# Optimization experiments

Measured on AMD Instinct MI355X. Metric: run time of the kernel, lower is better.

Reference implementation:

```python
import jax, jax.numpy as jnp
import numpy as np

# Static config (matches init_kwargs / docstring example)
SHAPES = ((100, 100), (50, 50), (25, 25), (13, 13))  # (H, W) per level
L, P, NH, HD, E, F = 4, 4, 8, 32, 256, 1024
NUM_LAYERS = 6
EPS = 1e-5
NUM_KEYS = sum(h * w for h, w in SHAPES)  # 13294


def _ln(x, g, b):
    m = jnp.mean(x, -1, keepdims=True)
    v = jnp.var(x, -1, keepdims=True)
    return (x - m) * jax.lax.rsqrt(v + EPS) * g + b


def _ms_deform_attn(value, loc, aw):
    # value: (B,N,NH,HD)  loc: (B,N,NH,L,P,2) normalized  aw: (B,N,NH,L,P)
    B, N = value.shape[:2]
    out = jnp.zeros((B, NH, N, HD), value.dtype)
    start = 0
    for lvl, (h, w) in enumerate(SHAPES):
        v = value[:, start:start + h * w].transpose(0, 2, 1, 3)  # (B,NH,hw,HD)
        start += h * w
        # grid_sample align_corners=False pixel coords
        x = loc[:, :, :, lvl, :, 0] * w - 0.5  # (B,N,NH,P)
        y = loc[:, :, :, lvl, :, 1] * h - 0.5
        x0 = jnp.floor(x); y0 = jnp.floor(y)
        lx = x - x0; ly = y - y0
        x0 = x0.astype(jnp.int32); y0 = y0.astype(jnp.int32)

        def gather(yi, xi):
            valid = ((xi >= 0) & (xi < w) & (yi >= 0) & (yi < h)).astype(value.dtype)
            idx = jnp.clip(yi, 0, h - 1) * w + jnp.clip(xi, 0, w - 1)  # (B,N,NH,P)
            idx = idx.transpose(0, 2, 1, 3).reshape(B, NH, N * P, 1)
            got = jnp.take_along_axis(v, idx, axis=2).reshape(B, NH, N, P, HD)
            return got * valid.transpose(0, 2, 1, 3)[..., None]

        def wgt(a):  # (B,N,NH,P) -> (B,NH,N,P,1)
            return a.transpose(0, 2, 1, 3)[..., None]

        samp = (gather(y0, x0) * wgt((1 - lx) * (1 - ly))
                + gather(y0, x0 + 1) * wgt(lx * (1 - ly))
                + gather(y0 + 1, x0) * wgt((1 - lx) * ly)
                + gather(y0 + 1, x0 + 1) * wgt(lx * ly))  # (B,NH,N,P,HD)
        out = out + jnp.sum(samp * wgt(aw[:, :, :, lvl]), axis=3)
    return out.transpose(0, 2, 1, 3).reshape(B, N, NH * HD)


def _layer(x, ref, Woff, boff, Waw, baw, Wv, bv, Wo, bo, ln1_g, ln1_b, Wf1, bf1, Wf2, bf2, ln2_g, ln2_b):
    B, N, _ = x.shape
    v = (x @ Wv + bv).reshape(B, N, NH, HD)
    off = (x @ Woff + boff).reshape(B, N, NH, L, P, 2)
    aw = jax.nn.softmax((x @ Waw + baw).reshape(B, N, NH, L * P), -1).reshape(B, N, NH, L, P)
    normalizer = jnp.asarray([[w, h] for (h, w) in SHAPES], x.dtype)  # (L,2) in (x,y)=(W,H)
    loc = ref[:, :, None, :, None, :] + off / normalizer[None, None, None, :, None, :]
    attn = _ms_deform_attn(v, loc, aw) @ Wo + bo
    x = _ln(x + attn, ln1_g, ln1_b)
    f = jax.nn.relu(x @ Wf1 + bf1) @ Wf2 + bf2
    return _ln(x + f, ln2_g, ln2_b)


def setup_inputs() -> dict:
    key = jax.random.key(0)
    ks = jax.random.split(key, 10)
    s = 0.02
    return {
        "src": jax.random.normal(ks[0], (2, NUM_KEYS, E), jnp.float32),
        "reference_points": jax.random.uniform(ks[1], (2, NUM_KEYS, L, 2), jnp.float32),
        "spatial_shapes": jnp.asarray(SHAPES, jnp.int32),
        "level_start_index": jnp.asarray([0, 10000, 12500, 13125], jnp.int32),
        "Woff": jax.random.normal(ks[2], (E, NH * L * P * 2), jnp.float32) * s,
        "boff": jnp.zeros((NH * L * P * 2,), jnp.float32),
        "Waw": jax.random.normal(ks[3], (E, NH * L * P), jnp.float32) * s,
        "baw": jnp.zeros((NH * L * P,), jnp.float32),
        "Wv": jax.random.normal(ks[4], (E, E), jnp.float32) * s,
        "bv": jnp.zeros((E,), jnp.float32),
        "Wo": jax.random.normal(ks[5], (E, E), jnp.float32) * s,
        "bo": jnp.zeros((E,), jnp.float32),
        "ln1_g": jnp.ones((E,), jnp.float32),
        "ln1_b": jnp.zeros((E,), jnp.float32),
        "Wf1": jax.random.normal(ks[6], (E, F), jnp.float32) * s,
        "bf1": jnp.zeros((F,), jnp.float32),
        "Wf2": jax.random.normal(ks[7], (F, E), jnp.float32) * s,
        "bf2": jnp.zeros((E,), jnp.float32),
        "ln2_g": jnp.ones((E,), jnp.float32),
        "ln2_b": jnp.zeros((E,), jnp.float32),
    }


def reference(src, reference_points, spatial_shapes, level_start_index, Woff, boff, Waw, baw, Wv, bv, Wo, bo, ln1_g, ln1_b, Wf1, bf1, Wf2, bf2, ln2_g, ln2_b):
    # NOTE: the torch encoder reuses the SAME layer object num_layers times,
    # so parameters are shared across all 6 layers.
    x = src
    for _ in range(NUM_LAYERS):
        x = _layer(x, reference_points, Woff, boff, Waw, baw, Wv, bv, Wo, bo,
                   ln1_g, ln1_b, Wf1, bf1, Wf2, bf2, ln2_g, ln2_b)
    return x
```

## Files before the change

kernel.cpp:

```cpp
#include <hip/hip_runtime.h>
#include <hip/hip_bf16.h>
#include <math.h>

#define NKEYS 13294
#define BATCH 2
#define MROWS (BATCH * NKEYS)
#define EDIM  256
#define FDIM  1024
#define EPSV  1e-5f

typedef __bf16 bf16x8 __attribute__((ext_vector_type(8)));
typedef float  f32x4  __attribute__((ext_vector_type(4)));
typedef float  f32x2  __attribute__((ext_vector_type(2)));

__device__ __forceinline__ void async16(const void* g, void* l) {
    __builtin_amdgcn_global_load_lds(
        (const __attribute__((address_space(1))) void*)g,
        (__attribute__((address_space(3))) void*)l, 16, 0, 0);
}

template<int MODE>
__global__ __launch_bounds__(256, 4) void gemm_mfma_k(
    const __hip_bfloat16* __restrict__ A, const __hip_bfloat16* __restrict__ WT,
    const float* __restrict__ bias, __hip_bfloat16* __restrict__ Cout,
    int M, int N, int K,
    __hip_bfloat16* __restrict__ o_vb, __hip_bfloat16* __restrict__ o_off,
    __hip_bfloat16* __restrict__ o_aw)
{
    constexpr int BM = 128, BN = 128, BKc = 32;
    constexpr int SMX = (BM + BN) * BKc;
    __shared__ __hip_bfloat16 smem[2 * SMX];

    const int gx = gridDim.x, nb = gx * gridDim.y;
    int bxi = blockIdx.x, byi = blockIdx.y;
    if ((nb & 7) == 0) {
        const int id   = byi * gx + bxi;
        const int tile = (id & 7) * (nb >> 3) + (id >> 3);
        bxi = tile % gx; byi = tile / gx;
    }
    const int bm = byi * BM;
    const int bn = bxi * BN;

    const int tid  = threadIdx.x;
    const int lane = tid & 63;
    const int w    = tid >> 6;
    const int wr   = w >> 1, wc = w & 1;
    const int l15  = lane & 15, quad = lane >> 4;

    const int gRow = tid >> 2;
    const int kc8  = (tid & 3) * 8;
    const __hip_bfloat16* gsrc[4];
    int ldsoff[4];
    #pragma unroll
    for (int rr = 0; rr < 4; ++rr) {
        const int gr = gRow + 64 * rr;
        if (gr < BM) {
            int ar = bm + gr; if (ar >= M) ar = M - 1;
            gsrc[rr] = A + (size_t)ar * K + kc8;
        } else {
            gsrc[rr] = WT + (size_t)(bn + gr - BM) * K + kc8;
        }
        ldsoff[rr] = gr * BKc + kc8;
    }

    f32x4 acc[4][4];
    #pragma unroll
    for (int i = 0; i < 4; ++i)
        #pragma unroll
        for (int j = 0; j < 4; ++j) acc[i][j] = (f32x4)0.f;

    const int T = K / BKc;
    #pragma unroll
    for (int rr = 0; rr < 4; ++rr) async16(gsrc[rr], smem + ldsoff[rr]);

    for (int it = 0; it < T; ++it) {
        __syncthreads();
        if (it + 1 < T) {
            const int nxt = ((it + 1) & 1) * SMX;
            const int ko  = (it + 1) * BKc;
            #pragma unroll
            for (int rr = 0; rr < 4; ++rr) async16(gsrc[rr] + ko, smem + nxt + ldsoff[rr]);
        }
        const __hip_bfloat16* sA = smem + (it & 1) * SMX;
        const __hip_bfloat16* sB = sA + BM * BKc;

        bf16x8 a[4], b[4];
        #pragma unroll
        for (int mt = 0; mt < 4; ++mt)
            a[mt] = *(const bf16x8*)&sA[(wr * 64 + mt * 16 + l15) * BKc + quad * 8];
        #pragma unroll
        for (int nt = 0; nt < 4; ++nt)
            b[nt] = *(const bf16x8*)&sB[(wc * 64 + nt * 16 + l15) * BKc + quad * 8];
        #pragma unroll
        for (int mt = 0; mt < 4; ++mt)
            #pragma unroll
            for (int nt = 0; nt < 4; ++nt)
                acc[mt][nt] = __builtin_amdgcn_mfma_f32_16x16x32_bf16(
                    b[nt], a[mt], acc[mt][nt], 0, 0, 0);
    }

    #pragma unroll
    for (int nt = 0; nt < 4; ++nt) {
        const int col = bn + wc * 64 + nt * 16 + quad * 4;
        const float4 bz = *(const float4*)&bias[col];
        #pragma unroll
        for (int mt = 0; mt < 4; ++mt) {
            const int row = bm + wr * 64 + mt * 16 + l15;
            if (row >= M) continue;
            float v0 = acc[mt][nt][0] + bz.x;
            float v1 = acc[mt][nt][1] + bz.y;
            float v2 = acc[mt][nt][2] + bz.z;
            float v3 = acc[mt][nt][3] + bz.w;
            if (MODE == 3) {
                v0 = fmaxf(v0, 0.f); v1 = fmaxf(v1, 0.f);
                v2 = fmaxf(v2, 0.f); v3 = fmaxf(v3, 0.f);
            }
            union { uint2 u; __hip_bfloat16 h[4]; } p;
            p.h[0] = __float2bfloat16(v0); p.h[1] = __float2bfloat16(v1);
            p.h[2] = __float2bfloat16(v2); p.h[3] = __float2bfloat16(v3);
            if (MODE == 1) {
                if (col < 256) {
                    const int bb = (row >= NKEYS) ? 1 : 0;
                    const int hh = col >> 5, d = col & 31;
                    *(uint2*)&o_vb[((size_t)(bb * 7 + hh) * NKEYS + row) * 32 + d] = p.u;
                } else if (col < 512) {
                    *(uint2*)&o_off[(size_t)row * 256 + (col - 256)] = p.u;
                } else {
                    *(uint2*)&o_aw[(size_t)row * 128 + (col - 512)] = p.u;
                }
            } else {
                *(uint2*)&Cout[(size_t)row * N + col] = p.u;
            }
        }
    }
}

template<int FINAL>
__global__ __launch_bounds__(256, 2) void gemm_ln_k(
    const __hip_bfloat16* __restrict__ A, const __hip_bfloat16* __restrict__ WT,
    const float* __restrict__ bias, const __hip_bfloat16* __restrict__ xres,
    const float* __restrict__ g, const float* __restrict__ bta,
    float* __restrict__ xfout, __hip_bfloat16* __restrict__ xbout,
    int M, int K)
{
    constexpr int BM = 64, BN = 256, BKc = 32;
    constexpr int ROWS = BM + BN;
    constexpr int SMX = ROWS * BKc;
    __shared__ __hip_bfloat16 smem[2 * SMX];

    const int tid  = threadIdx.x;
    const int bm   = blockIdx.x * BM;
    const int lane = tid & 63;
    const int w    = tid >> 6;
    const int l15  = lane & 15, quad = lane >> 4;

    const int gRow = tid >> 2;
    const int kc8  = (tid & 3) * 8;
    const __hip_bfloat16* gsrc[5];
    int ldsoff[5];
    #pragma unroll
    for (int rr = 0; rr < 5; ++rr) {
        const int gr = gRow + 64 * rr;
        if (gr < BM) {
            int ar = bm + gr; if (ar >= M) ar = M - 1;
            gsrc[rr] = A + (size_t)ar * K + kc8;
        } else {
            gsrc[rr] = WT + (size_t)(gr - BM) * K + kc8;
        }
        ldsoff[rr] = gr * BKc + kc8;
    }

    f32x4 acc[4][4];
    #pragma unroll
    for (int i = 0; i < 4; ++i)
        #pragma unroll
        for (int j = 0; j < 4; ++j) acc[i][j] = (f32x4)0.f;

    const int T = K / BKc;
    #pragma unroll
    for (int rr = 0; rr < 5; ++rr) async16(gsrc[rr], smem + ldsoff[rr]);

    for (int it = 0; it < T; ++it) {
        __syncthreads();
        if (it + 1 < T) {
            const int nxt = ((it + 1) & 1) * SMX;
            const int ko  = (it + 1) * BKc;
            #pragma unroll
            for (int rr = 0; rr < 5; ++rr) async16(gsrc[rr] + ko, smem + nxt + ldsoff[rr]);
        }
        const __hip_bfloat16* sA = smem + (it & 1) * SMX;
        const __hip_bfloat16* sB = sA + BM * BKc;

        bf16x8 a[4], b[4];
        #pragma unroll
        for (int mt = 0; mt < 4; ++mt)
            a[mt] = *(const bf16x8*)&sA[(mt * 16 + l15) * BKc + quad * 8];
        #pragma unroll
        for (int nt = 0; nt < 4; ++nt)
            b[nt] = *(const bf16x8*)&sB[(w * 64 + nt * 16 + l15) * BKc + quad * 8];
        #pragma unroll
        for (int mt = 0; mt < 4; ++mt)
            #pragma unroll
            for (int nt = 0; nt < 4; ++nt)
                acc[mt][nt] = __builtin_amdgcn_mfma_f32_16x16x32_bf16(
                    b[nt], a[mt], acc[mt][nt], 0, 0, 0);
    }

    const int colq = w * 64 + quad * 4;

    #pragma unroll
    for (int nt = 0; nt < 4; ++nt) {
        const int col = colq + nt * 16;
        const float4 bz = *(const float4*)&bias[col];
        #pragma unroll
        for (int mt = 0; mt < 4; ++mt) {
            int row = bm + mt * 16 + l15;
            if (row >= M) row = M - 1;
            const ushort4 xr = *(const ushort4*)&xres[(size_t)row * 256 + col];
            acc[mt][nt][0] += bz.x + __uint_as_float((unsigned)xr.x << 16);
            acc[mt][nt][1] += bz.y + __uint_as_float((unsigned)xr.y << 16);
            acc[mt][nt][2] += bz.z + __uint_as_float((unsigned)xr.z << 16);
            acc[mt][nt][3] += bz.w + __uint_as_float((unsigned)xr.w << 16);
        }
    }

    __syncthreads();
    float* stats = (float*)smem;
    #pragma unroll
    for (int mt = 0; mt < 4; ++mt) {
        float s = 0.f, sq = 0.f;
        #pragma unroll
        for (int nt = 0; nt < 4; ++nt)
            #pragma unroll
            for (int r = 0; r < 4; ++r) {
                const float v = acc[mt][nt][r];
                s += v; sq += v * v;
            }
        s  += __shfl_xor(s,  16, 64);  s  += __shfl_xor(s,  32, 64);
        sq += __shfl_xor(sq, 16, 64);  sq += __shfl_xor(sq, 32, 64);
        if (quad == 0) {
            const int rl = mt * 16 + l15;
            stats[(w * 64 + rl) * 2 + 0] = s;
            stats[(w * 64 + rl) * 2 + 1] = sq;
        }
    }
    __syncthreads();

    #pragma unroll
    for (int mt = 0; mt < 4; ++mt) {
        const int rl  = mt * 16 + l15;
        const int row = bm + rl;
        float s  = stats[rl * 2]          + stats[(64 + rl) * 2]
                 + stats[(128 + rl) * 2]  + stats[(192 + rl) * 2];
        float sq = stats[rl * 2 + 1]      + stats[(64 + rl) * 2 + 1]
                 + stats[(128 + rl) * 2 + 1] + stats[(192 + rl) * 2 + 1];
        const float mean = s * (1.f / 256.f);
        const float var  = sq * (1.f / 256.f) - mean * mean;
        const float rstd = rsqrtf(var + EPSV);
        if (row < M) {
            #pragma unroll
            for (int nt = 0; nt < 4; ++nt) {
                const int col = colq + nt * 16;
                const float4 gz  = *(const float4*)&g[col];
                const float4 bb4 = *(const float4*)&bta[col];
                const float v0 = (acc[mt][nt][0] - mean) * rstd * gz.x + bb4.x;
                const float v1 = (acc[mt][nt][1] - mean) * rstd * gz.y + bb4.y;
                const float v2 = (acc[mt][nt][2] - mean) * rstd * gz.z + bb4.z;
                const float v3 = (acc[mt][nt][3] - mean) * rstd * gz.w + bb4.w;
                union { uint2 u; __hip_bfloat16 h[4]; } p;
                p.h[0] = __float2bfloat16(v0); p.h[1] = __float2bfloat16(v1);
                p.h[2] = __float2bfloat16(v2); p.h[3] = __float2bfloat16(v3);
                *(uint2*)&xbout[(size_t)row * 256 + col] = p.u;
                if (FINAL) {
                    float4 f; f.x = v0; f.y = v1; f.z = v2; f.w = v3;
                    *(float4*)&xfout[(size_t)row * 256 + col] = f;
                }
            }
        }
    }
}

__global__ void convert_wt_k(const float* __restrict__ W, __hip_bfloat16* __restrict__ WT,
                             int K, int N, int rowOff)
{
    const int idx = blockIdx.x * 256 + threadIdx.x;
    if (idx >= K * N) return;
    const int k = idx / N, n = idx % N;
    WT[(size_t)(rowOff + n) * K + k] = __float2bfloat16(W[idx]);
}

__global__ void pack_bias_k(const float* __restrict__ bv, const float* __restrict__ boff,
                            const float* __restrict__ baw, float* __restrict__ dst)
{
    const int i = blockIdx.x * 256 + threadIdx.x;
    if (i < 256) dst[i] = bv[i];
    else if (i < 512) dst[i] = boff[i - 256];
    else if (i < 640) dst[i] = baw[i - 512];
}

__global__ void convert_src_k(const float* __restrict__ src, __hip_bfloat16* __restrict__ xb)
{
    const int i = blockIdx.x * 256 + threadIdx.x;
    const float4 v = ((const float4*)src)[i];
    xb[i * 4 + 0] = __float2bfloat16(v.x);
    xb[i * 4 + 1] = __float2bfloat16(v.y);
    xb[i * 4 + 2] = __float2bfloat16(v.z);
    xb[i * 4 + 3] = __float2bfloat16(v.w);
}

__global__ __launch_bounds__(256) void sample_k(
    const __hip_bfloat16* __restrict__ v_bf,
    const __hip_bfloat16* __restrict__ offb,
    const __hip_bfloat16* __restrict__ awb,
    const float* __restrict__ ref,
    __hip_bfloat16* __restrict__ out)
{
    __shared__ alignas(16) float sw[272][4];
    __shared__ alignas(16) int   sa[272][4];
    const int t  = threadIdx.x;
    const int q0 = blockIdx.x * 2;
    const int qi = t >> 7, h = (t >> 4) & 7;

    {
        const int i = t & 15;
        const int q = q0 + qi;
        const int l = i >> 2;
        const float logit = __bfloat162float(awb[(size_t)q * 128 + h * 16 + i]);
        float mx = logit;
        #pragma unroll
        for (int m = 1; m < 16; m <<= 1) mx = fmaxf(mx, __shfl_xor(mx, m, 64));
        const float e = __expf(logit - mx);
        float s = e;
        #pragma unroll
        for (int m = 1; m < 16; m <<= 1) s += __shfl_xor(s, m, 64);
        const float aw = e / s;

        const int ww = (l == 0) ? 100 : (l == 1) ? 50 : (l == 2) ? 25 : 13;
        const int ls = (l == 0) ? 0 : (l == 1) ? 10000 : (l == 2) ? 12500 : 13125;
        const int b  = (q >= NKEYS) ? 1 : 0;
        const int slab = (b * 8 + h) * NKEYS + ls;

        const __hip_bfloat162 ofp = *(const __hip_bfloat162*)&offb[(size_t)q * 256 + h * 32 + i * 2];
        const float2 rf = *(const float2*)&ref[(size_t)q * 8 + l * 2];
        const float x = rf.x * (float)ww + __bfloat162float(ofp.x) - 0.5f;
        const float y = rf.y * (float)ww + __bfloat162float(ofp.y) - 0.5f;
        const float x0f = floorf(x), y0f = floorf(y);
        const float lx = x - x0f, ly = y - y0f;
        const int x0 = (int)x0f, y0 = (int)y0f;
        const bool x0ok = (x0 >= 0) & (x0 < ww);
        const bool x1ok = (x0 + 1 >= 0) & (x0 + 1 < ww);
        const bool y0ok = (y0 >= 0) & (y0 < ww);
        const bool y1ok = (y0 + 1 >= 0) & (y0 + 1 < ww);

        float w00 = (1.f - lx) * (1.f - ly) * aw;
        float w01 = lx * (1.f - ly) * aw;
        float w10 = (1.f - lx) * ly * aw;
        float w11 = lx * ly * aw;
        int a00 = slab + y0 * ww + x0;
        int a01 = a00 + 1;
        int a10 = a00 + ww;
        int a11 = a10 + 1;
        if (!(y0ok & x0ok)) { w00 = 0.f; a00 = 0; }
        if (!(y0ok & x1ok)) { w01 = 0.f; a01 = 0; }
        if (!(y1ok & x0ok)) { w10 = 0.f; a10 = 0; }
        if (!(y1ok & x1ok)) { w11 = 0.f; a11 = 0; }

        const int idx = (qi * 8 + h) * 17 + i;
        sw[idx][0] = w00; sw[idx][1] = w01; sw[idx][2] = w10; sw[idx][3] = w11;
        sa[idx][0] = a00 * 64; sa[idx][1] = a01 * 64;
        sa[idx][2] = a10 * 64; sa[idx][3] = a11 * 64;
    }
    __syncthreads();

    const int d2 = t & 15;
    const unsigned d4 = d2 * 4;
    const char* vb = (const char*)v_bf;
    const int ebase = (qi * 8 + h) * 17;
    f32x2 acc = (f32x2)0.f;
    #pragma unroll
    for (int i = 0; i < 16; ++i) {
        const f32x4 wv = *(const f32x4*)sw[ebase + i];
        const int4  av = *(const int4*)sa[ebase + i];
        const unsigned p0 = *(const unsigned*)(vb + ((unsigned)av.x + d4));
        const unsigned p1 = *(const unsigned*)(vb + ((unsigned)av.y + d4));
        const unsigned p2 = *(const unsigned*)(vb + ((unsigned)av.z + d4));
        const unsigned p3 = *(const unsigned*)(vb + ((unsigned)av.w + d4));
        f32x2 v;
        v[0] = __uint_as_float(p0 << 16); v[1] = __uint_as_float(p0 & 0xffff0000u);
        acc += (f32x2)(wv[0]) * v;
        v[0] = __uint_as_float(p1 << 16); v[1] = __uint_as_float(p1 & 0xffff0000u);
        acc += (f32x2)(wv[1]) * v;
        v[0] = __uint_as_float(p2 << 16); v[1] = __uint_as_float(p2 & 0xffff0000u);
        acc += (f32x2)(wv[2]) * v;
        v[0] = __uint_as_float(p3 << 16); v[1] = __uint_as_float(p3 & 0xffff0000u);
        acc += (f32x2)(wv[3]) * v;
    }
    __hip_bfloat162 ov;
    ov.x = __float2bfloat16(acc[0]);
    ov.y = __float2bfloat16(acc[1]);
    *(__hip_bfloat162*)&out[(size_t)(q0 + qi) * 256 + h * 32 + d2 * 2] = ov;
}

extern "C" void kernel_launch(void* const* d_in, const int* in_sizes, int n_in,
                              void* d_out, int out_size, void* d_ws, size_t ws_size,
                              hipStream_t stream)
{
    const float* src  = (const float*)d_in[0];
    const float* ref  = (const float*)d_in[1];
    const float* Woff = (const float*)d_in[4];
    const float* boff = (const float*)d_in[5];
    const float* Waw  = (const float*)d_in[6];
    const float* baw  = (const float*)d_in[7];
    const float* Wv   = (const float*)d_in[8];
    const float* bv   = (const float*)d_in[9];
    const float* Wo   = (const float*)d_in[10];
    const float* bo   = (const float*)d_in[11];
    const float* ln1g = (const float*)d_in[12];
    const float* ln1b = (const float*)d_in[13];
    const float* Wf1  = (const float*)d_in[14];
    const float* bf1  = (const float*)d_in[15];
    const float* Wf2  = (const float*)d_in[16];
    const float* bf2  = (const float*)d_in[17];
    const float* ln2g = (const float*)d_in[18];
    const float* ln2b = (const float*)d_in[19];

    float* x = (float*)d_out;

    float* ws = (float*)d_ws;
    float* bias1 = ws;
    __hip_bfloat16* v_bf  = (__hip_bfloat16*)(bias1 + 640);
    __hip_bfloat16* offb  = v_bf  + (size_t)MROWS * 256;
    __hip_bfloat16* awb   = offb  + (size_t)MROWS * 256;
    __hip_bfloat16* xb    = awb   + (size_t)MROWS * 128;
    __hip_bfloat16* attnb = xb    + (size_t)MROWS * 256;
    __hip_bfloat16* hb    = attnb + (size_t)MROWS * 256;
    __hip_bfloat16* WT1   = hb    + (size_t)MROWS * 1024;
    __hip_bfloat16* WTo   = WT1   + 640 * 256;
    __hip_bfloat16* WTf1  = WTo   + 256 * 256;
    __hip_bfloat16* WTf2  = WTf1  + 1024 * 256;

    convert_wt_k<<<(256 * 256 + 255) / 256, 256, 0, stream>>>(Wv,   WT1,  256, 256,   0);
    convert_wt_k<<<(256 * 256 + 255) / 256, 256, 0, stream>>>(Woff, WT1,  256, 256, 256);
    convert_wt_k<<<(256 * 128 + 255) / 256, 256, 0, stream>>>(Waw,  WT1,  256, 128, 512);
    convert_wt_k<<<(256 * 256 + 255) / 256, 256, 0, stream>>>(Wo,   WTo,  256, 256,   0);
    convert_wt_k<<<(256 * 1024 + 255) / 256, 256, 0, stream>>>(Wf1, WTf1, 256, 1024,  0);
    convert_wt_k<<<(1024 * 256 + 255) / 256, 256, 0, stream>>>(Wf2, WTf2, 1024, 256,  0);
    pack_bias_k<<<3, 256, 0, stream>>>(bv, boff, baw, bias1);
    convert_src_k<<<(MROWS * 64 + 255) / 256, 256, 0, stream>>>(src, xb);

    const int gy  = (MROWS + 127) / 128;
    const int gln = (MROWS + 63) / 64;
    for (int layer = 0; layer < 6; ++layer) {
        gemm_mfma_k<1><<<dim3(640 / 128, gy), 256, 0, stream>>>(
            xb, WT1, bias1, nullptr, MROWS, 640, 256, v_bf, offb, awb);
        sample_k<<<MROWS / 2, 256, 0, stream>>>(v_bf, offb, awb, ref, attnb);
        gemm_ln_k<0><<<gln, 256, 0, stream>>>(
            attnb, WTo, bo, xb, ln1g, ln1b, nullptr, xb, MROWS, 256);
        gemm_mfma_k<3><<<dim3(1024 / 128, gy), 256, 0, stream>>>(
            xb, WTf1, bf1, hb, MROWS, 1024, 256, nullptr, nullptr, nullptr);
        if (layer < 5)
            gemm_ln_k<0><<<gln, 256, 0, stream>>>(
                hb, WTf2, bf2, xb, ln2g, ln2b, nullptr, xb, MROWS, 1024);
        else
            gemm_ln_k<1><<<gln, 256, 0, stream>>>(
                hb, WTf2, bf2, xb, ln2g, ln2b, x, xb, MROWS, 1024);
    }
}
```

Measured before the change: 1.049 ms.

## Fuse FFN up-projection, ReLU, down-projection and LayerNorm into one kernel

Replaces the separate FFN1 GEMM (which wrote a 1024-wide hidden buffer) and the FFN2 GEMM+LN kernel with one kernel per 64-row tile. It computes 64-column chunks of the hidden activation into double-buffered LDS and immediately accumulates them into the 256-wide output, then applies the residual and LayerNorm. This removes the large hidden tensor's global write and read. In exchange, each block streams both weight matrices directly from global memory without LDS staging, and it runs with lower occupancy (launch bounds 2) and a sync per chunk.

```diff
diff --git a/kernel.cpp b/kernel.cpp
--- a/kernel.cpp
+++ b/kernel.cpp
@@ -226,6 +226,173 @@
 
     __syncthreads();
     float* stats = (float*)smem;
+    #pragma unroll
+    for (int mt = 0; mt < 4; ++mt) {
+        float s = 0.f, sq = 0.f;
+        #pragma unroll
+        for (int nt = 0; nt < 4; ++nt)
+            #pragma unroll
+            for (int r = 0; r < 4; ++r) {
+                const float v = acc[mt][nt][r];
+                s += v; sq += v * v;
+            }
+        s  += __shfl_xor(s,  16, 64);  s  += __shfl_xor(s,  32, 64);
+        sq += __shfl_xor(sq, 16, 64);  sq += __shfl_xor(sq, 32, 64);
+        if (quad == 0) {
+            const int rl = mt * 16 + l15;
+            stats[(w * 64 + rl) * 2 + 0] = s;
+            stats[(w * 64 + rl) * 2 + 1] = sq;
+        }
+    }
+    __syncthreads();
+
+    #pragma unroll
+    for (int mt = 0; mt < 4; ++mt) {
+        const int rl  = mt * 16 + l15;
+        const int row = bm + rl;
+        float s  = stats[rl * 2]          + stats[(64 + rl) * 2]
+                 + stats[(128 + rl) * 2]  + stats[(192 + rl) * 2];
+        float sq = stats[rl * 2 + 1]      + stats[(64 + rl) * 2 + 1]
+                 + stats[(128 + rl) * 2 + 1] + stats[(192 + rl) * 2 + 1];
+        const float mean = s * (1.f / 256.f);
+        const float var  = sq * (1.f / 256.f) - mean * mean;
+        const float rstd = rsqrtf(var + EPSV);
+        if (row < M) {
+            #pragma unroll
+            for (int nt = 0; nt < 4; ++nt) {
+                const int col = colq + nt * 16;
+                const float4 gz  = *(const float4*)&g[col];
+                const float4 bb4 = *(const float4*)&bta[col];
+                const float v0 = (acc[mt][nt][0] - mean) * rstd * gz.x + bb4.x;
+                const float v1 = (acc[mt][nt][1] - mean) * rstd * gz.y + bb4.y;
+                const float v2 = (acc[mt][nt][2] - mean) * rstd * gz.z + bb4.z;
+                const float v3 = (acc[mt][nt][3] - mean) * rstd * gz.w + bb4.w;
+                union { uint2 u; __hip_bfloat16 h[4]; } p;
+                p.h[0] = __float2bfloat16(v0); p.h[1] = __float2bfloat16(v1);
+                p.h[2] = __float2bfloat16(v2); p.h[3] = __float2bfloat16(v3);
+                *(uint2*)&xbout[(size_t)row * 256 + col] = p.u;
+                if (FINAL) {
+                    float4 f; f.x = v0; f.y = v1; f.z = v2; f.w = v3;
+                    *(float4*)&xfout[(size_t)row * 256 + col] = f;
+                }
+            }
+        }
+    }
+}
+
+template<int FINAL>
+__global__ __launch_bounds__(256, 2) void ffn_fused_k(
+    const __hip_bfloat16* __restrict__ xin,
+    const __hip_bfloat16* __restrict__ WTf1,
+    const __hip_bfloat16* __restrict__ WTf2,
+    const float* __restrict__ bf1, const float* __restrict__ bf2,
+    const float* __restrict__ g, const float* __restrict__ bta,
+    float* __restrict__ xfout, __hip_bfloat16* __restrict__ xbout,
+    int M)
+{
+    __shared__ __hip_bfloat16 xs[8 * 64 * 32];
+    __shared__ __hip_bfloat16 ps[2 * 2 * 64 * 32];
+
+    const int tid  = threadIdx.x;
+    const int bm   = blockIdx.x * 64;
+    const int lane = tid & 63;
+    const int w    = tid >> 6;
+    const int l15  = lane & 15, quad = lane >> 4;
+
+    {
+        const int gr  = tid >> 2;
+        const int kc8 = (tid & 3) * 8;
+        int ar = bm + gr; if (ar >= M) ar = M - 1;
+        const __hip_bfloat16* src = xin + (size_t)ar * 256 + kc8;
+        #pragma unroll
+        for (int kt = 0; kt < 8; ++kt)
+            async16(src + kt * 32, xs + (kt * 64 + gr) * 32 + kc8);
+    }
+
+    f32x4 acc[4][4];
+    #pragma unroll
+    for (int i = 0; i < 4; ++i)
+        #pragma unroll
+        for (int j = 0; j < 4; ++j) acc[i][j] = (f32x4)0.f;
+
+    __syncthreads();
+
+    const int kt2w = w >> 1;
+    const int kcw  = (w & 1) * 16 + quad * 4;
+
+    for (int nf = 0; nf < 16; ++nf) {
+        const int buf = nf & 1;
+
+        bf16x8 bw[8];
+        {
+            const __hip_bfloat16* wp =
+                WTf1 + (size_t)(nf * 64 + w * 16 + l15) * 256 + quad * 8;
+            #pragma unroll
+            for (int kt = 0; kt < 8; ++kt) bw[kt] = *(const bf16x8*)(wp + kt * 32);
+        }
+        f32x4 pacc[4];
+        #pragma unroll
+        for (int mt = 0; mt < 4; ++mt) pacc[mt] = (f32x4)0.f;
+        #pragma unroll
+        for (int kt = 0; kt < 8; ++kt) {
+            #pragma unroll
+            for (int mt = 0; mt < 4; ++mt) {
+                const bf16x8 a = *(const bf16x8*)&xs[(kt * 64 + mt * 16 + l15) * 32 + quad * 8];
+                pacc[mt] = __builtin_amdgcn_mfma_f32_16x16x32_bf16(bw[kt], a, pacc[mt], 0, 0, 0);
+            }
+        }
+        {
+            const float4 bz = *(const float4*)&bf1[nf * 64 + w * 16 + quad * 4];
+            #pragma unroll
+            for (int mt = 0; mt < 4; ++mt) {
+                union { uint2 u; __hip_bfloat16 h[4]; } p;
+                p.h[0] = __float2bfloat16(fmaxf(pacc[mt][0] + bz.x, 0.f));
+                p.h[1] = __float2bfloat16(fmaxf(pacc[mt][1] + bz.y, 0.f));
+                p.h[2] = __float2bfloat16(fmaxf(pacc[mt][2] + bz.z, 0.f));
+                p.h[3] = __float2bfloat16(fmaxf(pacc[mt][3] + bz.w, 0.f));
+                *(uint2*)&ps[((buf * 2 + kt2w) * 64 + mt * 16 + l15) * 32 + kcw] = p.u;
+            }
+        }
+        __syncthreads();
+
+        const __hip_bfloat16* wp2 =
+            WTf2 + (size_t)(w * 64 + l15) * 1024 + nf * 64 + quad * 8;
+        #pragma unroll
+        for (int kt2 = 0; kt2 < 2; ++kt2) {
+            bf16x8 b2[4];
+            #pragma unroll
+            for (int nt = 0; nt < 4; ++nt)
+                b2[nt] = *(const bf16x8*)(wp2 + (size_t)nt * 16 * 1024 + kt2 * 32);
+            #pragma unroll
+            for (int mt = 0; mt < 4; ++mt) {
+                const bf16x8 a = *(const bf16x8*)&ps[((buf * 2 + kt2) * 64 + mt * 16 + l15) * 32 + quad * 8];
+                #pragma unroll
+                for (int nt = 0; nt < 4; ++nt)
+                    acc[mt][nt] = __builtin_amdgcn_mfma_f32_16x16x32_bf16(
+                        b2[nt], a, acc[mt][nt], 0, 0, 0);
+            }
+        }
+    }
+
+    const int colq = w * 64 + quad * 4;
+    #pragma unroll
+    for (int nt = 0; nt < 4; ++nt) {
+        const int col = colq + nt * 16;
+        const float4 bz = *(const float4*)&bf2[col];
+        const int ktr = col >> 5, kcr = col & 31;
+        #pragma unroll
+        for (int mt = 0; mt < 4; ++mt) {
+            const int row = mt * 16 + l15;
+            const ushort4 xr = *(const ushort4*)&xs[(ktr * 64 + row) * 32 + kcr];
+            acc[mt][nt][0] += bz.x + __uint_as_float((unsigned)xr.x << 16);
+            acc[mt][nt][1] += bz.y + __uint_as_float((unsigned)xr.y << 16);
+            acc[mt][nt][2] += bz.z + __uint_as_float((unsigned)xr.z << 16);
+            acc[mt][nt][3] += bz.w + __uint_as_float((unsigned)xr.w << 16);
+        }
+    }
+
+    __syncthreads();
+    float* stats = (float*)ps;
     #pragma unroll
     for (int mt = 0; mt < 4; ++mt) {
         float s = 0.f, sq = 0.f;
@@ -433,8 +600,7 @@
     __hip_bfloat16* awb   = offb  + (size_t)MROWS * 256;
     __hip_bfloat16* xb    = awb   + (size_t)MROWS * 128;
     __hip_bfloat16* attnb = xb    + (size_t)MROWS * 256;
-    __hip_bfloat16* hb    = attnb + (size_t)MROWS * 256;
-    __hip_bfloat16* WT1   = hb    + (size_t)MROWS * 1024;
+    __hip_bfloat16* WT1   = attnb + (size_t)MROWS * 256;
     __hip_bfloat16* WTo   = WT1   + 640 * 256;
     __hip_bfloat16* WTf1  = WTo   + 256 * 256;
     __hip_bfloat16* WTf2  = WTf1  + 1024 * 256;
@@ -456,13 +622,11 @@
         sample_k<<<MROWS / 2, 256, 0, stream>>>(v_bf, offb, awb, ref, attnb);
         gemm_ln_k<0><<<gln, 256, 0, stream>>>(
             attnb, WTo, bo, xb, ln1g, ln1b, nullptr, xb, MROWS, 256);
-        gemm_mfma_k<3><<<dim3(1024 / 128, gy), 256, 0, stream>>>(
-            xb, WTf1, bf1, hb, MROWS, 1024, 256, nullptr, nullptr, nullptr);
         if (layer < 5)
-            gemm_ln_k<0><<<gln, 256, 0, stream>>>(
-                hb, WTf2, bf2, xb, ln2g, ln2b, nullptr, xb, MROWS, 1024);
+            ffn_fused_k<0><<<gln, 256, 0, stream>>>(
+                xb, WTf1, WTf2, bf1, bf2, ln2g, ln2b, nullptr, xb, MROWS);
         else
-            gemm_ln_k<1><<<gln, 256, 0, stream>>>(
-                hb, WTf2, bf2, xb, ln2g, ln2b, x, xb, MROWS, 1024);
-    }
-}
+            ffn_fused_k<1><<<gln, 256, 0, stream>>>(
+                xb, WTf1, WTf2, bf1, bf2, ln2g, ln2b, x, xb, MROWS);
+    }
+}
```

Result: no change. 1.058 ms (+0.9%).
